# Kernel optimization log

Hardware: AMD Instinct MI355X
Metric: run time of the kernel (lower is better)

Reference implementation:

```python
import jax, jax.numpy as jnp
import numpy as np

B = 65536  # number of 32-bit words processed by the VM


def _build_tables():
    # ByteToNibbleFFN: byte one-hot -> (high, low) nibble one-hots
    W1_b2n = np.eye(256, dtype=np.float32)
    W2_b2n = np.zeros((256, 32), dtype=np.float32)
    for b in range(256):
        W2_b2n[b, (b >> 4) & 15] = 1.0
        W2_b2n[b, 16 + (b & 15)] = 1.0
    # NibbleToByteFFN: (high, low) -> byte one-hot
    W1_n2b = np.zeros((32, 256), dtype=np.float32)
    for high in range(16):
        for low in range(16):
            bv = (high << 4) | low
            W1_n2b[high, bv] = 1.0
            W1_n2b[16 + low, bv] = 1.0
    W2_n2b = np.eye(256, dtype=np.float32)
    # NibbleTableFFN for XOR
    W1_xor = np.zeros((32, 256), dtype=np.float32)
    W2_xor = np.zeros((256, 16), dtype=np.float32)
    for a in range(16):
        for b in range(16):
            k = a * 16 + b
            W1_xor[a, k] = 1.0
            W1_xor[16 + b, k] = 1.0
            W2_xor[k, (a ^ b) & 15] = 1.0
    # NibbleAddFFN: (a, b, carry) -> (sum, carry)
    W1_add = np.zeros((34, 512), dtype=np.float32)
    W2_sum = np.zeros((512, 16), dtype=np.float32)
    W2_carry = np.zeros((512, 2), dtype=np.float32)
    for a in range(16):
        for b in range(16):
            for c in range(2):
                k = a * 32 + b * 2 + c
                W1_add[a, k] = 1.0
                W1_add[16 + b, k] = 1.0
                W1_add[32 + c, k] = 1.0
                total = a + b + c
                W2_sum[k, total & 15] = 1.0
                W2_carry[k, 1 if total >= 16 else 0] = 1.0
    return (jnp.asarray(W1_b2n), jnp.asarray(W2_b2n), jnp.asarray(W1_n2b),
            jnp.asarray(W2_n2b), jnp.asarray(W1_xor), jnp.asarray(W2_xor),
            jnp.asarray(W1_add), jnp.asarray(W2_sum), jnp.asarray(W2_carry))


def setup_inputs() -> dict:
    key = jax.random.key(0)
    k1, k2 = jax.random.split(key)
    a_idx = jax.random.randint(k1, (B, 4), 0, 256)
    b_idx = jax.random.randint(k2, (B, 4), 0, 256)
    a_bytes = jax.nn.one_hot(a_idx, 256, dtype=jnp.float32)  # [B,4,256]
    b_bytes = jax.nn.one_hot(b_idx, 256, dtype=jnp.float32)
    (W1_b2n, W2_b2n, W1_n2b, W2_n2b, W1_xor, W2_xor,
     W1_add, W2_sum, W2_carry) = _build_tables()
    return {
        'a_bytes': a_bytes, 'b_bytes': b_bytes,
        'W1_b2n': W1_b2n, 'W2_b2n': W2_b2n,
        'W1_n2b': W1_n2b, 'W2_n2b': W2_n2b,
        'W1_xor': W1_xor, 'W2_xor': W2_xor,
        'W1_add': W1_add, 'W2_sum': W2_sum, 'W2_carry': W2_carry,
    }


def reference(a_bytes, b_bytes, W1_b2n, W2_b2n, W1_n2b, W2_n2b,
              W1_xor, W2_xor, W1_add, W2_sum, W2_carry):
    # Batched faithful translation of the torch VM: the torch code loops over
    # single words; here each op is vectorized over the word batch B while the
    # fixed 4-byte carry chain remains an explicit (structural) loop.
    def byte_to_nib(x):                       # x: [B,256]
        w = jax.nn.softmax((x @ W1_b2n) * 100.0, axis=-1)
        nib = w @ W2_b2n                      # [B,32]
        return nib[:, :16], nib[:, 16:]

    def nib_to_byte(high, low):               # [B,16] each -> [B,256]
        x = jnp.concatenate([high, low], axis=-1)
        w = jax.nn.softmax((x @ W1_n2b - 1.5) * 20.0, axis=-1)
        return w @ W2_n2b

    def nib_xor(a, b):                        # [B,16] each -> [B,16]
        x = jnp.concatenate([a, b], axis=-1)
        w = jax.nn.softmax((x @ W1_xor - 1.5) * 20.0, axis=-1)
        return w @ W2_xor

    def nib_add(a, b, c):                     # [B,16],[B,16],[B,2]
        x = jnp.concatenate([a, b, c], axis=-1)
        w = jax.nn.softmax((x @ W1_add - 2.5) * 20.0, axis=-1)
        return w @ W2_sum, w @ W2_carry

    def byte_xor(a, b):                       # [B,256] each
        a_h, a_l = byte_to_nib(a)
        b_h, b_l = byte_to_nib(b)
        return nib_to_byte(nib_xor(a_h, b_h), nib_xor(a_l, b_l))

    n = a_bytes.shape[0]
    # ByteAddFFN: 4-byte ripple-carry add, carry starts as one-hot 0
    carry = jnp.broadcast_to(jnp.array([1.0, 0.0], dtype=a_bytes.dtype), (n, 2))
    sum_bytes = []
    for i in range(4):
        a_h, a_l = byte_to_nib(a_bytes[:, i])
        b_h, b_l = byte_to_nib(b_bytes[:, i])
        r_low, carry_low = nib_add(a_l, b_l, carry)
        r_high, carry = nib_add(a_h, b_h, carry_low)
        sum_bytes.append(nib_to_byte(r_high, r_low))
    # Chain a second VM op: XOR the sum with operand a, per byte
    out = [byte_xor(sum_bytes[i], a_bytes[:, i]) for i in range(4)]
    return jnp.stack(out, axis=1)             # [B,4,256]
```

## Files before the change

### kernel.cpp

```cpp
#include <hip/hip_runtime.h>
#include <stdint.h>

typedef float f32x4 __attribute__((ext_vector_type(4)));

__global__ __launch_bounds__(256) void vm_kernel(
    const float* __restrict__ a_bytes,
    const float* __restrict__ b_bytes,
    float* __restrict__ out,
    int n_words)
{
    const int lane = threadIdx.x & 63;
    const int w    = blockIdx.x * 4 + (threadIdx.x >> 6);
    if (w >= n_words) return;

    const long base = (long)w * 1024 + lane * 4;
    const float* pa = a_bytes + base;
    const float* pb = b_bytes + base;

    const f32x4 a0 = *(const f32x4*)(pa);
    const f32x4 a1 = *(const f32x4*)(pa + 256);
    const f32x4 a2 = *(const f32x4*)(pa + 512);
    const f32x4 a3 = *(const f32x4*)(pa + 768);
    const f32x4 b0 = *(const f32x4*)(pb);
    const f32x4 b1 = *(const f32x4*)(pb + 256);
    const f32x4 b2 = *(const f32x4*)(pb + 512);
    const f32x4 b3 = *(const f32x4*)(pb + 768);

    auto idx_of = [&](const f32x4 v) -> uint32_t {
        const uint64_t m0 = __ballot(v.x > 0.5f);
        const uint64_t m1 = __ballot(v.y > 0.5f);
        const uint64_t m2 = __ballot(v.z > 0.5f);
        const uint64_t m3 = __ballot(v.w > 0.5f);
        const uint64_t m  = m0 | m1 | m2 | m3;
        const uint32_t hl = (uint32_t)__ffsll((unsigned long long)m) - 1u;
        const uint32_t c  = (m1 ? 1u : 0u) | (m2 ? 2u : 0u) | (m3 ? 3u : 0u);
        return hl * 4u + c;
    };

    const uint32_t aw = idx_of(a0) | (idx_of(a1) << 8) |
                        (idx_of(a2) << 16) | (idx_of(a3) << 24);
    const uint32_t bw = idx_of(b0) | (idx_of(b1) << 8) |
                        (idx_of(b2) << 16) | (idx_of(b3) << 24);

    const uint32_t s = aw + bw;
    const uint32_t o = s ^ aw;

    float* po = out + base;
    const int j = lane * 4;
#pragma unroll
    for (int k = 0; k < 4; ++k) {
        const int oi = (int)((o >> (8 * k)) & 255u);
        f32x4 ov;
        ov.x = (j     == oi) ? 1.0f : 0.0f;
        ov.y = (j + 1 == oi) ? 1.0f : 0.0f;
        ov.z = (j + 2 == oi) ? 1.0f : 0.0f;
        ov.w = (j + 3 == oi) ? 1.0f : 0.0f;
        *(f32x4*)(po + k * 256) = ov;
    }
}

extern "C" void kernel_launch(void* const* d_in, const int* in_sizes, int n_in,
                              void* d_out, int out_size, void* d_ws, size_t ws_size,
                              hipStream_t stream)
{
    const float* a_bytes = (const float*)d_in[0];
    const float* b_bytes = (const float*)d_in[1];
    float* out = (float*)d_out;
    const int n_words = in_sizes[0] / 1024;

    const int blocks = (n_words + 3) / 4;
    vm_kernel<<<blocks, 256, 0, stream>>>(a_bytes, b_bytes, out, n_words);
}
```

Baseline: 591.6 us.

## Split fused kernel into read-decode and write-expand phases via workspace

New measurement: 597.4 us. Within noise of the previous version (+1.0%).

```diff
diff --git a/kernel.cpp b/kernel.cpp
--- a/kernel.cpp
+++ b/kernel.cpp
@@ -3,7 +3,75 @@
 
 typedef float f32x4 __attribute__((ext_vector_type(4)));
 
-__global__ __launch_bounds__(256) void vm_kernel(
+__global__ __launch_bounds__(256) void vm_phase1(
+    const float* __restrict__ a_bytes,
+    const float* __restrict__ b_bytes,
+    uint32_t* __restrict__ ws,
+    int n_words)
+{
+    const int lane = threadIdx.x & 63;
+    const int w    = blockIdx.x * 4 + (threadIdx.x >> 6);
+    if (w >= n_words) return;
+
+    const long base = (long)w * 1024 + lane * 4;
+    const float* pa = a_bytes + base;
+    const float* pb = b_bytes + base;
+
+    const f32x4 a0 = *(const f32x4*)(pa);
+    const f32x4 a1 = *(const f32x4*)(pa + 256);
+    const f32x4 a2 = *(const f32x4*)(pa + 512);
+    const f32x4 a3 = *(const f32x4*)(pa + 768);
+    const f32x4 b0 = *(const f32x4*)(pb);
+    const f32x4 b1 = *(const f32x4*)(pb + 256);
+    const f32x4 b2 = *(const f32x4*)(pb + 512);
+    const f32x4 b3 = *(const f32x4*)(pb + 768);
+
+    auto idx_of = [&](const f32x4 v) -> uint32_t {
+        const uint64_t m0 = __ballot(v.x > 0.5f);
+        const uint64_t m1 = __ballot(v.y > 0.5f);
+        const uint64_t m2 = __ballot(v.z > 0.5f);
+        const uint64_t m3 = __ballot(v.w > 0.5f);
+        const uint64_t m  = m0 | m1 | m2 | m3;
+        const uint32_t hl = (uint32_t)__ffsll((unsigned long long)m) - 1u;
+        const uint32_t c  = (m1 ? 1u : 0u) | (m2 ? 2u : 0u) | (m3 ? 3u : 0u);
+        return hl * 4u + c;
+    };
+
+    const uint32_t aw = idx_of(a0) | (idx_of(a1) << 8) |
+                        (idx_of(a2) << 16) | (idx_of(a3) << 24);
+    const uint32_t bw = idx_of(b0) | (idx_of(b1) << 8) |
+                        (idx_of(b2) << 16) | (idx_of(b3) << 24);
+    const uint32_t s = aw + bw;
+    const uint32_t o = s ^ aw;
+
+    if (lane == 0) ws[w] = o;
+}
+
+__global__ __launch_bounds__(256) void vm_phase2(
+    const uint32_t* __restrict__ ws,
+    float* __restrict__ out,
+    int n_words)
+{
+    const int lane = threadIdx.x & 63;
+    const int w    = blockIdx.x * 4 + (threadIdx.x >> 6);
+    if (w >= n_words) return;
+
+    const uint32_t o = ws[w];
+    float* po = out + (long)w * 1024 + lane * 4;
+    const int j = lane * 4;
+#pragma unroll
+    for (int k = 0; k < 4; ++k) {
+        const int oi = (int)((o >> (8 * k)) & 255u);
+        f32x4 ov;
+        ov.x = (j     == oi) ? 1.0f : 0.0f;
+        ov.y = (j + 1 == oi) ? 1.0f : 0.0f;
+        ov.z = (j + 2 == oi) ? 1.0f : 0.0f;
+        ov.w = (j + 3 == oi) ? 1.0f : 0.0f;
+        *(f32x4*)(po + k * 256) = ov;
+    }
+}
+
+__global__ __launch_bounds__(256) void vm_fused(
     const float* __restrict__ a_bytes,
     const float* __restrict__ b_bytes,
     float* __restrict__ out,
@@ -41,7 +109,6 @@
                         (idx_of(a2) << 16) | (idx_of(a3) << 24);
     const uint32_t bw = idx_of(b0) | (idx_of(b1) << 8) |
                         (idx_of(b2) << 16) | (idx_of(b3) << 24);
-
     const uint32_t s = aw + bw;
     const uint32_t o = s ^ aw;
 
@@ -67,7 +134,13 @@
     const float* b_bytes = (const float*)d_in[1];
     float* out = (float*)d_out;
     const int n_words = in_sizes[0] / 1024;
+    const int blocks  = (n_words + 3) / 4;
 
-    const int blocks = (n_words + 3) / 4;
-    vm_kernel<<<blocks, 256, 0, stream>>>(a_bytes, b_bytes, out, n_words);
+    if (d_ws != nullptr && ws_size >= (size_t)n_words * 4) {
+        uint32_t* ws = (uint32_t*)d_ws;
+        vm_phase1<<<blocks, 256, 0, stream>>>(a_bytes, b_bytes, ws, n_words);
+        vm_phase2<<<blocks, 256, 0, stream>>>(ws, out, n_words);
+    } else {
+        vm_fused<<<blocks, 256, 0, stream>>>(a_bytes, b_bytes, out, n_words);
+    }
 }
```
